# Performance work log

Measured on AMD Instinct MI355X. Metric: run time of the kernel, lower is better.

The kernel has to match this reference:

```python
import jax, jax.numpy as jnp
import numpy as np

N_NODES = 50000
N_EDGES = 800000
IN_FEATS = 256
HIDDEN = 128
OUT_FEATS = 64


def setup_inputs() -> dict:
    key = jax.random.key(0)
    k1, k2, k3, k4, k5 = jax.random.split(key, 5)
    x = jax.random.normal(k1, (N_NODES, IN_FEATS), dtype=jnp.float32)
    src = jax.random.randint(k2, (N_EDGES,), 0, N_NODES, dtype=jnp.int64)
    dst = jax.random.randint(k3, (N_EDGES,), 0, N_NODES, dtype=jnp.int64)
    # Glorot-ish init for linear weights (DGL GraphConv uses xavier_uniform)
    W1 = jax.random.normal(k4, (IN_FEATS, HIDDEN), dtype=jnp.float32) / np.sqrt(IN_FEATS)
    W2 = jax.random.normal(k5, (HIDDEN, OUT_FEATS), dtype=jnp.float32) / np.sqrt(HIDDEN)
    b1 = jnp.zeros((HIDDEN,), dtype=jnp.float32)
    b2 = jnp.zeros((OUT_FEATS,), dtype=jnp.float32)
    return {"x": x, "src": src, "dst": dst, "W1": W1, "b1": b1, "W2": W2, "b2": b2}


def _norms(src, dst, n_nodes):
    ones = jnp.ones(src.shape[0], dtype=jnp.float32)
    deg_out = jax.ops.segment_sum(ones, src, num_segments=n_nodes)
    deg_in = jax.ops.segment_sum(ones, dst, num_segments=n_nodes)
    # DGL clamps zero degrees to 1 to avoid inf
    norm_src = jnp.power(jnp.clip(deg_out, 1.0, None), -0.5)  # [N]
    norm_dst = jnp.power(jnp.clip(deg_in, 1.0, None), -0.5)   # [N]
    return norm_src, norm_dst


def _gcn_layer(h, W, b, src, dst, norm_src, norm_dst, n_nodes):
    # norm='both': D_dst^{-1/2} A D_src^{-1/2} (h W) + b
    # multiply by W first (in_feats >= out_feats -> cheaper aggregation)
    m = (h * norm_src[:, None]) @ W            # [N, out]
    agg = jax.ops.segment_sum(m[src], dst, num_segments=n_nodes)  # [N, out]
    return agg * norm_dst[:, None] + b


def reference(x, src, dst, W1, b1, W2, b2):
    n = x.shape[0]
    norm_src, norm_dst = _norms(src, dst, n)
    h = _gcn_layer(x, W1, b1, src, dst, norm_src, norm_dst, n)
    h = jax.nn.relu(h)
    h = _gcn_layer(h, W2, b2, src, dst, norm_src, norm_dst, n)
    return h
```

## Files before the change

### kernel.cpp

```cpp
#include <hip/hip_runtime.h>

#define N_NODES 50000
#define N_EDGES 800000
#define IN_FEATS 256
#define HIDDEN 128
#define OUT_FEATS 64

#define NB 8192
#define NRANGE 7
#define NBT (NRANGE * NB)
#define NCHUNK 64
#define EPC 12500
#define HBLK (NRANGE * NCHUNK)
#define ROWBLK ((N_NODES + 63) / 64)

typedef _Float16 f16;
typedef _Float16 f16x2 __attribute__((ext_vector_type(2)));
typedef _Float16 f16x8 __attribute__((ext_vector_type(8)));
typedef float f32x4 __attribute__((ext_vector_type(4)));

__global__ __launch_bounds__(256) void hist_gemm_kernel(
    const int* __restrict__ src, const int* __restrict__ dst,
    unsigned* __restrict__ hist_src, unsigned* __restrict__ hist_dst,
    const float* __restrict__ W1, const float* __restrict__ W2,
    f16* __restrict__ W2T, const float* __restrict__ x,
    f16* __restrict__ m1) {
  __shared__ __align__(16) unsigned smem[8192];
  if (blockIdx.x < HBLK) {
    unsigned* ls = smem;
    unsigned* ld2 = smem + NB / 2;
    const int r = blockIdx.x % NRANGE;
    const int c = blockIdx.x / NRANGE;
    const int lo = r * NB;
    for (int i = threadIdx.x; i < NB / 2; i += 256) {
      ls[i] = 0;
      ld2[i] = 0;
    }
    __syncthreads();
    const int4* s4 = (const int4*)(src + c * EPC);
    const int4* d4 = (const int4*)(dst + c * EPC);
    for (int i = threadIdx.x; i < EPC / 4; i += 256) {
      int4 s = s4[i];
      int4 d = d4[i];
      unsigned b;
      b = (unsigned)(s.x - lo); if (b < NB) atomicAdd(&ls[b >> 1], 1u << ((b & 1) << 4));
      b = (unsigned)(s.y - lo); if (b < NB) atomicAdd(&ls[b >> 1], 1u << ((b & 1) << 4));
      b = (unsigned)(s.z - lo); if (b < NB) atomicAdd(&ls[b >> 1], 1u << ((b & 1) << 4));
      b = (unsigned)(s.w - lo); if (b < NB) atomicAdd(&ls[b >> 1], 1u << ((b & 1) << 4));
      b = (unsigned)(d.x - lo); if (b < NB) atomicAdd(&ld2[b >> 1], 1u << ((b & 1) << 4));
      b = (unsigned)(d.y - lo); if (b < NB) atomicAdd(&ld2[b >> 1], 1u << ((b & 1) << 4));
      b = (unsigned)(d.z - lo); if (b < NB) atomicAdd(&ld2[b >> 1], 1u << ((b & 1) << 4));
      b = (unsigned)(d.w - lo); if (b < NB) atomicAdd(&ld2[b >> 1], 1u << ((b & 1) << 4));
    }
    __syncthreads();
    unsigned* hs = hist_src + ((long)c * NBT + lo) / 2;
    unsigned* hd = hist_dst + ((long)c * NBT + lo) / 2;
    for (int i = threadIdx.x; i < NB / 2; i += 256) {
      hs[i] = ls[i];
      hd[i] = ld2[i];
    }
    if (blockIdx.x < 32) {
      int j = blockIdx.x * 256 + threadIdx.x;
      int n = j >> 7, k = j & 127;
      W2T[j] = (f16)W2[k * 64 + n];
    }
  } else {
    char* BsBytes = (char*)smem;
    const int rb = blockIdx.x - HBLK;
    const int wave = threadIdx.x >> 6;
    const int lane = threadIdx.x & 63;
    const int m = lane & 15;
    const int q = lane >> 4;
    const int row0 = rb * 64 + wave * 16;
    const int ra = min(row0 + m, N_NODES - 1);

    f16x8 a[8];
#pragma unroll
    for (int ki = 0; ki < 8; ++ki) {
      const float* p = x + (long)ra * IN_FEATS + ki * 32 + q * 8;
      float4 u0 = *(const float4*)p;
      float4 u1 = *(const float4*)(p + 4);
      a[ki][0] = (f16)u0.x; a[ki][1] = (f16)u0.y;
      a[ki][2] = (f16)u0.z; a[ki][3] = (f16)u0.w;
      a[ki][4] = (f16)u1.x; a[ki][5] = (f16)u1.y;
      a[ki][6] = (f16)u1.z; a[ki][7] = (f16)u1.w;
    }

    for (int h = 0; h < 2; ++h) {
      const int col0 = h * 64;
      for (int idx = threadIdx.x; idx < 64 * 128; idx += 256) {
        int k2 = idx >> 6;
        int n = idx & 63;
        float a0 = W1[(2 * k2) * HIDDEN + col0 + n];
        float a1 = W1[(2 * k2 + 1) * HIDDEN + col0 + n];
        f16x2 pk;
        pk[0] = (f16)a0;
        pk[1] = (f16)a1;
        unsigned bo = (unsigned)(n * 512 + 4 * k2);
        bo ^= (unsigned)((n & 7) << 4);
        *(f16x2*)(BsBytes + bo) = pk;
      }
      __syncthreads();

      f32x4 acc[4];
#pragma unroll
      for (int t = 0; t < 4; ++t) acc[t] = (f32x4){0.f, 0.f, 0.f, 0.f};

#pragma unroll
      for (int ki = 0; ki < 8; ++ki) {
        const int kb2 = (ki * 32 + q * 8) * 2;
#pragma unroll
        for (int t = 0; t < 4; ++t) {
          int nrow = t * 16 + m;
          unsigned bo = (unsigned)(nrow * 512 + kb2);
          bo ^= (unsigned)((nrow & 7) << 4);
          f16x8 bfr = *(const f16x8*)(BsBytes + bo);
          acc[t] = __builtin_amdgcn_mfma_f32_16x16x32_f16(a[ki], bfr, acc[t], 0, 0, 0);
        }
      }
      __syncthreads();

#pragma unroll
      for (int rr = 0; rr < 4; ++rr) {
        int row = row0 + q * 4 + rr;
        if (row < N_NODES) {
#pragma unroll
          for (int t = 0; t < 4; ++t)
            m1[(long)row * HIDDEN + col0 + t * 16 + m] = (f16)acc[t][rr];
        }
      }
    }
  }
}

__global__ __launch_bounds__(256) void reduce_kernel(
    const unsigned* __restrict__ hist_src, unsigned* __restrict__ hist_dst,
    int* __restrict__ deg_in, float* __restrict__ norm_src,
    float* __restrict__ norm_dst, int* __restrict__ partial) {
  const unsigned short* hs = (const unsigned short*)hist_src;
  unsigned short* hd = (unsigned short*)hist_dst;
  int n = blockIdx.x * 256 + threadIdx.x;
  int run = 0;
  if (n < N_NODES) {
    int so = 0;
#pragma unroll 8
    for (int c = 0; c < NCHUNK; ++c) so += hs[(long)c * NBT + n];
    norm_src[n] = rsqrtf((float)max(so, 1));
#pragma unroll 8
    for (int c = 0; c < NCHUNK; ++c) {
      int t = hd[(long)c * NBT + n];
      hd[(long)c * NBT + n] = (unsigned short)run;
      run += t;
    }
    deg_in[n] = run;
    norm_dst[n] = rsqrtf((float)max(run, 1));
  }
  __shared__ int sd[256];
  sd[threadIdx.x] = run;
  __syncthreads();
  for (int s = 128; s > 0; s >>= 1) {
    if (threadIdx.x < s) sd[threadIdx.x] += sd[threadIdx.x + s];
    __syncthreads();
  }
  if (threadIdx.x == 0) partial[blockIdx.x] = sd[0];
}

__global__ __launch_bounds__(256) void scan3(const int* __restrict__ deg,
                                             const int* __restrict__ partial,
                                             int* __restrict__ rowptr) {
  __shared__ int sd[256];
  __shared__ int sp[256];
  const int w = blockIdx.x;
  int pv = (threadIdx.x < 196) ? partial[threadIdx.x] : 0;
  sp[threadIdx.x] = pv;
  __syncthreads();
  for (int off = 1; off < 256; off <<= 1) {
    int t = sp[threadIdx.x] +
            ((threadIdx.x >= off) ? sp[threadIdx.x - off] : 0);
    __syncthreads();
    sp[threadIdx.x] = t;
    __syncthreads();
  }
  const int base = (w == 0) ? 0 : sp[w - 1];
  int i = w * 256 + threadIdx.x;
  int v = (i < N_NODES) ? deg[i] : 0;
  sd[threadIdx.x] = v;
  __syncthreads();
  for (int off = 1; off < 256; off <<= 1) {
    int t = sd[threadIdx.x] +
            ((threadIdx.x >= off) ? sd[threadIdx.x - off] : 0);
    __syncthreads();
    sd[threadIdx.x] = t;
    __syncthreads();
  }
  if (i < N_NODES) rowptr[i] = base + sd[threadIdx.x] - v;
  if (w == 0 && threadIdx.x == 0) rowptr[N_NODES] = N_EDGES;
}

__global__ __launch_bounds__(256) void fill_csr(
    const int* __restrict__ src, const int* __restrict__ dst,
    const int* __restrict__ rowptr, const unsigned* __restrict__ pref32,
    int* __restrict__ col) {
  __shared__ int cur[NB];
  const unsigned short* pref = (const unsigned short*)pref32;
  const int r = blockIdx.x % NRANGE;
  const int c = blockIdx.x / NRANGE;
  const int lo = r * NB;
  for (int i = threadIdx.x; i < NB; i += 256) {
    int n = lo + i;
    cur[i] = (n < N_NODES) ? rowptr[n] + pref[(long)c * NBT + n] : 0;
  }
  __syncthreads();
  const int4* s4 = (const int4*)(src + c * EPC);
  const int4* d4 = (const int4*)(dst + c * EPC);
  for (int i = threadIdx.x; i < EPC / 4; i += 256) {
    int4 s = s4[i];
    int4 d = d4[i];
    unsigned b;
    b = (unsigned)(d.x - lo);
    if (b < NB) col[atomicAdd(&cur[b], 1)] = s.x;
    b = (unsigned)(d.y - lo);
    if (b < NB) col[atomicAdd(&cur[b], 1)] = s.y;
    b = (unsigned)(d.z - lo);
    if (b < NB) col[atomicAdd(&cur[b], 1)] = s.z;
    b = (unsigned)(d.w - lo);
    if (b < NB) col[atomicAdd(&cur[b], 1)] = s.w;
  }
}

template <int K, int NC, int TN, bool FP32IN>
__global__ __launch_bounds__(256) void gemm_mfma(
    const void* __restrict__ Xv, const f16* __restrict__ WT,
    const float* __restrict__ ns, f16* __restrict__ Mout) {
  constexpr int KI = K / 32;
  constexpr int COLBLK = NC / (TN * 16);
  constexpr int KP = K + 8;
  __shared__ f16 Bs[TN * 16 * KP];

  const int cb = blockIdx.x % COLBLK;
  const int rb = blockIdx.x / COLBLK;
  const int col0 = cb * TN * 16;
  const int wave = threadIdx.x >> 6;
  const int lane = threadIdx.x & 63;
  const int m = lane & 15;
  const int q = lane >> 4;
  const int row0 = rb * 64 + wave * 16;

  for (int idx = threadIdx.x; idx < TN * 16 * (K / 8); idx += 256) {
    int n = idx / (K / 8);
    int kk = idx % (K / 8);
    *(f16x8*)(Bs + n * KP + kk * 8) =
        *(const f16x8*)(WT + (long)(col0 + n) * K + kk * 8);
  }
  __syncthreads();

  const int ra = min(row0 + m, N_NODES - 1);
  const float s = FP32IN ? ns[ra] : 0.f;

  f32x4 acc[TN];
#pragma unroll
  for (int t = 0; t < TN; ++t) acc[t] = (f32x4){0.f, 0.f, 0.f, 0.f};

#pragma unroll
  for (int ki = 0; ki < KI; ++ki) {
    const int kb = ki * 32 + q * 8;
    f16x8 a;
    if (FP32IN) {
      const float* X = (const float*)Xv;
      const float* p = X + (long)ra * K + kb;
      float4 u0 = *(const float4*)p;
      float4 u1 = *(const float4*)(p + 4);
      a[0] = (f16)(u0.x * s); a[1] = (f16)(u0.y * s);
      a[2] = (f16)(u0.z * s); a[3] = (f16)(u0.w * s);
      a[4] = (f16)(u1.x * s); a[5] = (f16)(u1.y * s);
      a[6] = (f16)(u1.z * s); a[7] = (f16)(u1.w * s);
    } else {
      const f16* X = (const f16*)Xv;
      a = *(const f16x8*)(X + (long)ra * K + kb);
    }
#pragma unroll
    for (int t = 0; t < TN; ++t) {
      f16x8 b = *(const f16x8*)(Bs + (t * 16 + m) * KP + kb);
      acc[t] = __builtin_amdgcn_mfma_f32_16x16x32_f16(a, b, acc[t], 0, 0, 0);
    }
  }

#pragma unroll
  for (int r = 0; r < 4; ++r) {
    int row = row0 + q * 4 + r;
    if (row < N_NODES) {
#pragma unroll
      for (int t = 0; t < TN; ++t)
        Mout[(long)row * NC + col0 + t * 16 + m] = (f16)acc[t][r];
    }
  }
}

__global__ __launch_bounds__(256) void gather1_kernel(
    const f16* __restrict__ M, const int* __restrict__ rowptr,
    const int* __restrict__ col, const float* __restrict__ nd,
    const float* __restrict__ ns, const float* __restrict__ b,
    f16* __restrict__ out) {
  constexpr int LPR = 16;
  constexpr int EPW = 64 / LPR;
  const int wave = threadIdx.x >> 6;
  const int lane = threadIdx.x & 63;
  const int eg = lane / LPR;
  const int t = lane % LPR;
  const int n = blockIdx.x * 4 + wave;
  if (n >= N_NODES) return;
  const int beg = rowptr[n];
  const int end = rowptr[n + 1];

  float acc[8];
#pragma unroll
  for (int j = 0; j < 8; ++j) acc[j] = 0.f;

  int i = beg + eg;
  for (; i + EPW < end; i += 2 * EPW) {
    int s0 = col[i];
    int s1 = col[i + EPW];
    float n0 = ns[s0];
    float n1 = ns[s1];
    f16x8 v0 = *(const f16x8*)(M + (long)s0 * HIDDEN + t * 8);
    f16x8 v1 = *(const f16x8*)(M + (long)s1 * HIDDEN + t * 8);
#pragma unroll
    for (int j = 0; j < 8; ++j)
      acc[j] += n0 * (float)v0[j] + n1 * (float)v1[j];
  }
  if (i < end) {
    int s0 = col[i];
    float n0 = ns[s0];
    f16x8 v0 = *(const f16x8*)(M + (long)s0 * HIDDEN + t * 8);
#pragma unroll
    for (int j = 0; j < 8; ++j) acc[j] += n0 * (float)v0[j];
  }

#pragma unroll
  for (int m2 = LPR; m2 < 64; m2 <<= 1)
#pragma unroll
    for (int j = 0; j < 8; ++j) acc[j] += __shfl_xor(acc[j], m2, 64);

  if (eg == 0) {
    float s = nd[n];
    float sn = ns[n];
    float4 bb0 = *(const float4*)(b + t * 8);
    float4 bb1 = *(const float4*)(b + t * 8 + 4);
    f16x8 o;
    o[0] = (f16)(fmaxf(acc[0] * s + bb0.x, 0.f) * sn);
    o[1] = (f16)(fmaxf(acc[1] * s + bb0.y, 0.f) * sn);
    o[2] = (f16)(fmaxf(acc[2] * s + bb0.z, 0.f) * sn);
    o[3] = (f16)(fmaxf(acc[3] * s + bb0.w, 0.f) * sn);
    o[4] = (f16)(fmaxf(acc[4] * s + bb1.x, 0.f) * sn);
    o[5] = (f16)(fmaxf(acc[5] * s + bb1.y, 0.f) * sn);
    o[6] = (f16)(fmaxf(acc[6] * s + bb1.z, 0.f) * sn);
    o[7] = (f16)(fmaxf(acc[7] * s + bb1.w, 0.f) * sn);
    *(f16x8*)(out + (long)n * HIDDEN + t * 8) = o;
  }
}

__global__ __launch_bounds__(256) void gather2_kernel(
    const f16* __restrict__ M, const int* __restrict__ rowptr,
    const int* __restrict__ col, const float* __restrict__ nd,
    const float* __restrict__ b, float* __restrict__ out) {
  constexpr int LPR = 8;
  constexpr int EPW = 64 / LPR;
  const int wave = threadIdx.x >> 6;
  const int lane = threadIdx.x & 63;
  const int eg = lane / LPR;
  const int t = lane % LPR;
  const int n = blockIdx.x * 4 + wave;
  if (n >= N_NODES) return;
  const int beg = rowptr[n];
  const int end = rowptr[n + 1];

  float acc[8];
#pragma unroll
  for (int j = 0; j < 8; ++j) acc[j] = 0.f;

  int i = beg + eg;
  for (; i + EPW < end; i += 2 * EPW) {
    int s0 = col[i];
    int s1 = col[i + EPW];
    f16x8 v0 = *(const f16x8*)(M + (long)s0 * OUT_FEATS + t * 8);
    f16x8 v1 = *(const f16x8*)(M + (long)s1 * OUT_FEATS + t * 8);
#pragma unroll
    for (int j = 0; j < 8; ++j) acc[j] += (float)v0[j] + (float)v1[j];
  }
  if (i < end) {
    int s0 = col[i];
    f16x8 v0 = *(const f16x8*)(M + (long)s0 * OUT_FEATS + t * 8);
#pragma unroll
    for (int j = 0; j < 8; ++j) acc[j] += (float)v0[j];
  }

#pragma unroll
  for (int m2 = LPR; m2 < 64; m2 <<= 1)
#pragma unroll
    for (int j = 0; j < 8; ++j) acc[j] += __shfl_xor(acc[j], m2, 64);

  if (eg == 0) {
    float s = nd[n];
    float4 bb0 = *(const float4*)(b + t * 8);
    float4 bb1 = *(const float4*)(b + t * 8 + 4);
    float4 o0, o1;
    o0.x = acc[0] * s + bb0.x;
    o0.y = acc[1] * s + bb0.y;
    o0.z = acc[2] * s + bb0.z;
    o0.w = acc[3] * s + bb0.w;
    o1.x = acc[4] * s + bb1.x;
    o1.y = acc[5] * s + bb1.y;
    o1.z = acc[6] * s + bb1.z;
    o1.w = acc[7] * s + bb1.w;
    *(float4*)(out + (long)n * OUT_FEATS + t * 8) = o0;
    *(float4*)(out + (long)n * OUT_FEATS + t * 8 + 4) = o1;
  }
}

extern "C" void kernel_launch(void* const* d_in, const int* in_sizes, int n_in,
                              void* d_out, int out_size, void* d_ws,
                              size_t ws_size, hipStream_t stream) {
  const float* x = (const float*)d_in[0];
  const int* src = (const int*)d_in[1];
  const int* dst = (const int*)d_in[2];
  const float* W1 = (const float*)d_in[3];
  const float* b1 = (const float*)d_in[4];
  const float* W2 = (const float*)d_in[5];
  const float* b2 = (const float*)d_in[6];
  float* out = (float*)d_out;

  int* wi = (int*)d_ws;
  int* partial = wi;
  int* rowptr = wi + 256;
  int* deg_in = wi + 50260;
  int* col = wi + 100260;
  float* wf = (float*)d_ws + 900260;
  float* norm_src = wf;
  float* norm_dst = wf + 50000;
  f16* fh = (f16*)(wf + 100000);
  f16* W2T = fh;
  f16* m1 = fh + 64 * 128;
  f16* h1p = m1 + (long)50048 * 128;
  f16* m2 = h1p + (long)50048 * 128;

  unsigned* hist_src = (unsigned*)h1p;
  unsigned* hist_dst = hist_src + (long)NCHUNK * NBT / 2;

  const int nb_nodes = (N_NODES + 255) / 256;

  hist_gemm_kernel<<<HBLK + ROWBLK, 256, 0, stream>>>(
      src, dst, hist_src, hist_dst, W1, W2, W2T, x, m1);
  reduce_kernel<<<nb_nodes, 256, 0, stream>>>(hist_src, hist_dst, deg_in,
                                              norm_src, norm_dst, partial);
  scan3<<<nb_nodes, 256, 0, stream>>>(deg_in, partial, rowptr);
  fill_csr<<<HBLK, 256, 0, stream>>>(src, dst, rowptr, hist_dst, col);

  gather1_kernel<<<(N_NODES + 3) / 4, 256, 0, stream>>>(m1, rowptr, col,
                                                        norm_dst, norm_src, b1,
                                                        h1p);

  gemm_mfma<HIDDEN, OUT_FEATS, 4, false>
      <<<ROWBLK, 256, 0, stream>>>(h1p, W2T, norm_src, m2);
  gather2_kernel<<<(N_NODES + 3) / 4, 256, 0, stream>>>(m2, rowptr, col,
                                                        norm_dst, b2, out);
}
```

Measured before the change: 226.8 us.

## Use 8-bit chunk histograms and pretransposed f16 W1 read directly in GEMM

Histogram counters shrink from 16 to 8 bits, so each block covers 16384 nodes and only 4 ranges are launched, which halves histogram storage and blocks. A separate kernel transposes and converts W1 and W2 to f16 up front. The fused GEMM then loads B fragments directly from global memory, computing all 128 columns in one pass without LDS staging or barriers. The 8-bit per-chunk counts assume no node receives 256 or more edges within one chunk, and the direct global loads rely on cache hits.

```diff
diff --git a/kernel.cpp b/kernel.cpp
--- a/kernel.cpp
+++ b/kernel.cpp
@@ -6,33 +6,49 @@
 #define HIDDEN 128
 #define OUT_FEATS 64
 
-#define NB 8192
-#define NRANGE 7
-#define NBT (NRANGE * NB)
 #define NCHUNK 64
 #define EPC 12500
-#define HBLK (NRANGE * NCHUNK)
+#define NBH 16384
+#define NRH 4
+#define NBTH (NRH * NBH)
+#define HBLKH (NRH * NCHUNK)
+#define NBF 8192
+#define NRF 7
+#define FBLK (NRF * NCHUNK)
 #define ROWBLK ((N_NODES + 63) / 64)
 
 typedef _Float16 f16;
-typedef _Float16 f16x2 __attribute__((ext_vector_type(2)));
 typedef _Float16 f16x8 __attribute__((ext_vector_type(8)));
 typedef float f32x4 __attribute__((ext_vector_type(4)));
+
+__global__ __launch_bounds__(256) void wtrans(const float* __restrict__ W1,
+                                              const float* __restrict__ W2,
+                                              f16* __restrict__ W1T,
+                                              f16* __restrict__ W2T) {
+  int i = blockIdx.x * 256 + threadIdx.x;
+  if (i < 128 * 256) {
+    int n = i >> 8, k = i & 255;
+    W1T[i] = (f16)W1[k * 128 + n];
+  } else {
+    int j = i - 128 * 256;
+    int n = j >> 7, k = j & 127;
+    W2T[j] = (f16)W2[k * 64 + n];
+  }
+}
 
 __global__ __launch_bounds__(256) void hist_gemm_kernel(
     const int* __restrict__ src, const int* __restrict__ dst,
     unsigned* __restrict__ hist_src, unsigned* __restrict__ hist_dst,
-    const float* __restrict__ W1, const float* __restrict__ W2,
-    f16* __restrict__ W2T, const float* __restrict__ x,
+    const f16* __restrict__ W1T, const float* __restrict__ x,
     f16* __restrict__ m1) {
-  __shared__ __align__(16) unsigned smem[8192];
-  if (blockIdx.x < HBLK) {
+  __shared__ unsigned smem[8192];
+  if (blockIdx.x < HBLKH) {
     unsigned* ls = smem;
-    unsigned* ld2 = smem + NB / 2;
-    const int r = blockIdx.x % NRANGE;
-    const int c = blockIdx.x / NRANGE;
-    const int lo = r * NB;
-    for (int i = threadIdx.x; i < NB / 2; i += 256) {
+    unsigned* ld2 = smem + NBH / 4;
+    const int r = blockIdx.x % NRH;
+    const int c = blockIdx.x / NRH;
+    const int lo = r * NBH;
+    for (int i = threadIdx.x; i < NBH / 4; i += 256) {
       ls[i] = 0;
       ld2[i] = 0;
     }
@@ -43,30 +59,24 @@
       int4 s = s4[i];
       int4 d = d4[i];
       unsigned b;
-      b = (unsigned)(s.x - lo); if (b < NB) atomicAdd(&ls[b >> 1], 1u << ((b & 1) << 4));
-      b = (unsigned)(s.y - lo); if (b < NB) atomicAdd(&ls[b >> 1], 1u << ((b & 1) << 4));
-      b = (unsigned)(s.z - lo); if (b < NB) atomicAdd(&ls[b >> 1], 1u << ((b & 1) << 4));
-      b = (unsigned)(s.w - lo); if (b < NB) atomicAdd(&ls[b >> 1], 1u << ((b & 1) << 4));
-      b = (unsigned)(d.x - lo); if (b < NB) atomicAdd(&ld2[b >> 1], 1u << ((b & 1) << 4));
-      b = (unsigned)(d.y - lo); if (b < NB) atomicAdd(&ld2[b >> 1], 1u << ((b & 1) << 4));
-      b = (unsigned)(d.z - lo); if (b < NB) atomicAdd(&ld2[b >> 1], 1u << ((b & 1) << 4));
-      b = (unsigned)(d.w - lo); if (b < NB) atomicAdd(&ld2[b >> 1], 1u << ((b & 1) << 4));
-    }
-    __syncthreads();
-    unsigned* hs = hist_src + ((long)c * NBT + lo) / 2;
-    unsigned* hd = hist_dst + ((long)c * NBT + lo) / 2;
-    for (int i = threadIdx.x; i < NB / 2; i += 256) {
+      b = (unsigned)(s.x - lo); if (b < NBH) atomicAdd(&ls[b >> 2], 1u << ((b & 3) << 3));
+      b = (unsigned)(s.y - lo); if (b < NBH) atomicAdd(&ls[b >> 2], 1u << ((b & 3) << 3));
+      b = (unsigned)(s.z - lo); if (b < NBH) atomicAdd(&ls[b >> 2], 1u << ((b & 3) << 3));
+      b = (unsigned)(s.w - lo); if (b < NBH) atomicAdd(&ls[b >> 2], 1u << ((b & 3) << 3));
+      b = (unsigned)(d.x - lo); if (b < NBH) atomicAdd(&ld2[b >> 2], 1u << ((b & 3) << 3));
+      b = (unsigned)(d.y - lo); if (b < NBH) atomicAdd(&ld2[b >> 2], 1u << ((b & 3) << 3));
+      b = (unsigned)(d.z - lo); if (b < NBH) atomicAdd(&ld2[b >> 2], 1u << ((b & 3) << 3));
+      b = (unsigned)(d.w - lo); if (b < NBH) atomicAdd(&ld2[b >> 2], 1u << ((b & 3) << 3));
+    }
+    __syncthreads();
+    unsigned* hs = hist_src + ((long)c * NBTH + lo) / 4;
+    unsigned* hd = hist_dst + ((long)c * NBTH + lo) / 4;
+    for (int i = threadIdx.x; i < NBH / 4; i += 256) {
       hs[i] = ls[i];
       hd[i] = ld2[i];
     }
-    if (blockIdx.x < 32) {
-      int j = blockIdx.x * 256 + threadIdx.x;
-      int n = j >> 7, k = j & 127;
-      W2T[j] = (f16)W2[k * 64 + n];
-    }
   } else {
-    char* BsBytes = (char*)smem;
-    const int rb = blockIdx.x - HBLK;
+    const int rb = blockIdx.x - HBLKH;
     const int wave = threadIdx.x >> 6;
     const int lane = threadIdx.x & 63;
     const int m = lane & 15;
@@ -86,48 +96,27 @@
       a[ki][6] = (f16)u1.z; a[ki][7] = (f16)u1.w;
     }
 
-    for (int h = 0; h < 2; ++h) {
-      const int col0 = h * 64;
-      for (int idx = threadIdx.x; idx < 64 * 128; idx += 256) {
-        int k2 = idx >> 6;
-        int n = idx & 63;
-        float a0 = W1[(2 * k2) * HIDDEN + col0 + n];
-        float a1 = W1[(2 * k2 + 1) * HIDDEN + col0 + n];
-        f16x2 pk;
-        pk[0] = (f16)a0;
-        pk[1] = (f16)a1;
-        unsigned bo = (unsigned)(n * 512 + 4 * k2);
-        bo ^= (unsigned)((n & 7) << 4);
-        *(f16x2*)(BsBytes + bo) = pk;
+    f32x4 acc[8];
+#pragma unroll
+    for (int t = 0; t < 8; ++t) acc[t] = (f32x4){0.f, 0.f, 0.f, 0.f};
+
+#pragma unroll
+    for (int ki = 0; ki < 8; ++ki) {
+      const int kb = ki * 32 + q * 8;
+#pragma unroll
+      for (int t = 0; t < 8; ++t) {
+        f16x8 bfr = *(const f16x8*)(W1T + (t * 16 + m) * IN_FEATS + kb);
+        acc[t] = __builtin_amdgcn_mfma_f32_16x16x32_f16(a[ki], bfr, acc[t], 0, 0, 0);
       }
-      __syncthreads();
-
-      f32x4 acc[4];
-#pragma unroll
-      for (int t = 0; t < 4; ++t) acc[t] = (f32x4){0.f, 0.f, 0.f, 0.f};
-
-#pragma unroll
-      for (int ki = 0; ki < 8; ++ki) {
-        const int kb2 = (ki * 32 + q * 8) * 2;
-#pragma unroll
-        for (int t = 0; t < 4; ++t) {
-          int nrow = t * 16 + m;
-          unsigned bo = (unsigned)(nrow * 512 + kb2);
-          bo ^= (unsigned)((nrow & 7) << 4);
-          f16x8 bfr = *(const f16x8*)(BsBytes + bo);
-          acc[t] = __builtin_amdgcn_mfma_f32_16x16x32_f16(a[ki], bfr, acc[t], 0, 0, 0);
-        }
-      }
-      __syncthreads();
-
-#pragma unroll
-      for (int rr = 0; rr < 4; ++rr) {
-        int row = row0 + q * 4 + rr;
-        if (row < N_NODES) {
-#pragma unroll
-          for (int t = 0; t < 4; ++t)
-            m1[(long)row * HIDDEN + col0 + t * 16 + m] = (f16)acc[t][rr];
-        }
+    }
+
+#pragma unroll
+    for (int rr = 0; rr < 4; ++rr) {
+      int row = row0 + q * 4 + rr;
+      if (row < N_NODES) {
+#pragma unroll
+        for (int t = 0; t < 8; ++t)
+          m1[(long)row * HIDDEN + t * 16 + m] = (f16)acc[t][rr];
       }
     }
   }
@@ -137,19 +126,19 @@
     const unsigned* __restrict__ hist_src, unsigned* __restrict__ hist_dst,
     int* __restrict__ deg_in, float* __restrict__ norm_src,
     float* __restrict__ norm_dst, int* __restrict__ partial) {
-  const unsigned short* hs = (const unsigned short*)hist_src;
-  unsigned short* hd = (unsigned short*)hist_dst;
+  const unsigned char* hs = (const unsigned char*)hist_src;
+  unsigned char* hd = (unsigned char*)hist_dst;
   int n = blockIdx.x * 256 + threadIdx.x;
   int run = 0;
   if (n < N_NODES) {
     int so = 0;
 #pragma unroll 8
-    for (int c = 0; c < NCHUNK; ++c) so += hs[(long)c * NBT + n];
+    for (int c = 0; c < NCHUNK; ++c) so += hs[(long)c * NBTH + n];
     norm_src[n] = rsqrtf((float)max(so, 1));
 #pragma unroll 8
     for (int c = 0; c < NCHUNK; ++c) {
-      int t = hd[(long)c * NBT + n];
-      hd[(long)c * NBT + n] = (unsigned short)run;
+      int t = hd[(long)c * NBTH + n];
+      hd[(long)c * NBTH + n] = (unsigned char)run;
       run += t;
     }
     deg_in[n] = run;
@@ -201,14 +190,14 @@
     const int* __restrict__ src, const int* __restrict__ dst,
     const int* __restrict__ rowptr, const unsigned* __restrict__ pref32,
     int* __restrict__ col) {
-  __shared__ int cur[NB];
-  const unsigned short* pref = (const unsigned short*)pref32;
-  const int r = blockIdx.x % NRANGE;
-  const int c = blockIdx.x / NRANGE;
-  const int lo = r * NB;
-  for (int i = threadIdx.x; i < NB; i += 256) {
+  __shared__ int cur[NBF];
+  const unsigned char* pref = (const unsigned char*)pref32;
+  const int r = blockIdx.x % NRF;
+  const int c = blockIdx.x / NRF;
+  const int lo = r * NBF;
+  for (int i = threadIdx.x; i < NBF; i += 256) {
     int n = lo + i;
-    cur[i] = (n < N_NODES) ? rowptr[n] + pref[(long)c * NBT + n] : 0;
+    cur[i] = (n < N_NODES) ? rowptr[n] + pref[(long)c * NBTH + n] : 0;
   }
   __syncthreads();
   const int4* s4 = (const int4*)(src + c * EPC);
@@ -218,13 +207,13 @@
     int4 d = d4[i];
     unsigned b;
     b = (unsigned)(d.x - lo);
-    if (b < NB) col[atomicAdd(&cur[b], 1)] = s.x;
+    if (b < NBF) col[atomicAdd(&cur[b], 1)] = s.x;
     b = (unsigned)(d.y - lo);
-    if (b < NB) col[atomicAdd(&cur[b], 1)] = s.y;
+    if (b < NBF) col[atomicAdd(&cur[b], 1)] = s.y;
     b = (unsigned)(d.z - lo);
-    if (b < NB) col[atomicAdd(&cur[b], 1)] = s.z;
+    if (b < NBF) col[atomicAdd(&cur[b], 1)] = s.z;
     b = (unsigned)(d.w - lo);
-    if (b < NB) col[atomicAdd(&cur[b], 1)] = s.w;
+    if (b < NBF) col[atomicAdd(&cur[b], 1)] = s.w;
   }
 }
 
@@ -438,22 +427,24 @@
   float* norm_src = wf;
   float* norm_dst = wf + 50000;
   f16* fh = (f16*)(wf + 100000);
-  f16* W2T = fh;
-  f16* m1 = fh + 64 * 128;
+  f16* W1T = fh;
+  f16* W2T = fh + 128 * 256;
+  f16* m1 = W2T + 64 * 128;
   f16* h1p = m1 + (long)50048 * 128;
   f16* m2 = h1p + (long)50048 * 128;
 
   unsigned* hist_src = (unsigned*)h1p;
-  unsigned* hist_dst = hist_src + (long)NCHUNK * NBT / 2;
+  unsigned* hist_dst = hist_src + (long)NCHUNK * NBTH / 4;
 
   const int nb_nodes = (N_NODES + 255) / 256;
 
-  hist_gemm_kernel<<<HBLK + ROWBLK, 256, 0, stream>>>(
-      src, dst, hist_src, hist_dst, W1, W2, W2T, x, m1);
+  wtrans<<<160, 256, 0, stream>>>(W1, W2, W1T, W2T);
+  hist_gemm_kernel<<<HBLKH + ROWBLK, 256, 0, stream>>>(
+      src, dst, hist_src, hist_dst, W1T, x, m1);
   reduce_kernel<<<nb_nodes, 256, 0, stream>>>(hist_src, hist_dst, deg_in,
                                               norm_src, norm_dst, partial);
   scan3<<<nb_nodes, 256, 0, stream>>>(deg_in, partial, rowptr);
-  fill_csr<<<HBLK, 256, 0, stream>>>(src, dst, rowptr, hist_dst, col);
+  fill_csr<<<FBLK, 256, 0, stream>>>(src, dst, rowptr, hist_dst, col);
 
   gather1_kernel<<<(N_NODES + 3) / 4, 256, 0, stream>>>(m1, rowptr, col,
                                                         norm_dst, norm_src, b1,
```

After: 238.6 us. 5.2% more time.
